# Kernel tuning notes

Measured on AMD Instinct MI355X. Metric: run time of the kernel, lower is better.

## Reference

```python
import jax, jax.numpy as jnp
import numpy as np

UNITS = 256
D_IN = 256


def setup_inputs() -> dict:
    key = jax.random.key(0)
    ks = jax.random.split(key, 12)
    B, T, M, d, u = 16, 128, 512, D_IN, UNITS
    s = lambda fan_in: 1.0 / np.sqrt(fan_in)
    return {
        "inputs": jax.random.normal(ks[0], (B, T, d), jnp.float32),
        "attended_inputs": jax.random.normal(ks[1], (B, M, d), jnp.float32),
        # key_dense: Dense(units) applied to attended_inputs
        "key_W": jax.random.normal(ks[2], (d, u), jnp.float32) * s(d),
        "key_b": jnp.zeros((u,), jnp.float32),
        # query_dense: Dense(units) applied to state_h
        "query_W": jax.random.normal(ks[3], (u, u), jnp.float32) * s(u),
        "query_b": jnp.zeros((u,), jnp.float32),
        # attention_dense: Dense(1)
        "attn_W": jax.random.normal(ks[4], (u, 1), jnp.float32) * s(u),
        "attn_b": jnp.zeros((1,), jnp.float32),
        # LSTMCell built with input dim 2*d (inputs concat context); gate order i,f,g,o
        "lstm_W": jax.random.normal(ks[5], (2 * d, 4 * u), jnp.float32) * s(2 * d),
        "lstm_U": jax.random.normal(ks[6], (u, 4 * u), jnp.float32) * s(u),
        "lstm_b": jnp.zeros((4 * u,), jnp.float32),
    }


def reference(inputs, attended_inputs, key_W, key_b, query_W, query_b,
              attn_W, attn_b, lstm_W, lstm_U, lstm_b):
    B, T, d = inputs.shape
    u = lstm_U.shape[0]
    # keys computed once, shared across all timesteps: [B, M, u]
    keys = jnp.einsum('bmd,du->bmu', attended_inputs, key_W) + key_b
    aw = attn_W[:, 0]  # [u]

    def step(carry, x_t):
        h, c = carry                                   # [B,u], [B,u]
        q = h @ query_W + query_b                      # [B,u]
        e = jnp.tanh(keys + q[:, None, :])             # [B,M,u]
        scores = jnp.einsum('bmu,u->bm', e, aw) + attn_b[0]
        a = jax.nn.softmax(scores, axis=-1)            # [B,M]
        ctx = jnp.einsum('bm,bmd->bd', a, attended_inputs)
        xin = jnp.concatenate([x_t, ctx], axis=-1)     # [B,2d]
        z = xin @ lstm_W + h @ lstm_U + lstm_b         # [B,4u]
        i_g, f_g, g_g, o_g = jnp.split(z, 4, axis=-1)
        i_g = jax.nn.sigmoid(i_g)
        f_g = jax.nn.sigmoid(f_g)
        g_g = jnp.tanh(g_g)
        o_g = jax.nn.sigmoid(o_g)
        c_new = f_g * c + i_g * g_g
        h_new = o_g * jnp.tanh(c_new)
        return (h_new, c_new), h_new

    h0 = jnp.zeros((B, u), inputs.dtype)
    c0 = jnp.zeros((B, u), inputs.dtype)
    (hT, cT), ys = jax.lax.scan(step, (h0, c0), jnp.swapaxes(inputs, 0, 1))
    seq = jnp.swapaxes(ys, 0, 1)  # [B,T,u] (return_sequences=True)
    return seq, hT, cT
```

## Files before the change

### kernel.cpp

```cpp
#include <hip/hip_runtime.h>
#include <hip/hip_bf16.h>
#include <cstddef>

#define BATCH 16
#define TSTEPS 128
#define MSLOTS 512
#define DIN 256
#define UNITS 256
#define ZDIM 1024
#define G 8
#define NBLK (BATCH*G)
#define NTHR 1024

static __device__ __forceinline__ float tanhf_fast(float x) {
    float e = __expf(2.0f * x);
    return 1.0f - 2.0f / (e + 1.0f);
}
static __device__ __forceinline__ float sigmoidf_fast(float x) {
    return 1.0f / (1.0f + __expf(-x));
}
static __device__ __forceinline__ void st_agent_u(unsigned* p, unsigned v) {
    __hip_atomic_store(p, v, __ATOMIC_RELAXED, __HIP_MEMORY_SCOPE_AGENT);
}
static __device__ __forceinline__ unsigned ld_agent_u(const unsigned* p) {
    return __hip_atomic_load(p, __ATOMIC_RELAXED, __HIP_MEMORY_SCOPE_AGENT);
}
static __device__ __forceinline__ unsigned pack_bf(float a, float b) {
    unsigned ua = __float_as_uint(a); ua = (ua + 0x7fffu + ((ua >> 16) & 1u)) >> 16;
    unsigned ub = __float_as_uint(b); ub = ((ub + 0x7fffu + ((ub >> 16) & 1u)) >> 16) << 16;
    return ua | ub;
}
static __device__ __forceinline__ float bf_lo(unsigned w) { return __uint_as_float(w << 16); }
static __device__ __forceinline__ float bf_hi(unsigned w) { return __uint_as_float(w & 0xffff0000u); }

__global__ __launch_bounds__(256) void gemm_bias_kernel(
    const float* __restrict__ A, const float* __restrict__ B,
    const float* __restrict__ bias, float* __restrict__ C,
    int M, int N, int K)
{
    __shared__ float As[16][68];
    __shared__ float Bs[16][68];
    const int tid = threadIdx.x;
    const int bm = blockIdx.x * 64;
    const int bn = blockIdx.y * 64;
    const int tx = tid & 15, ty = tid >> 4;
    const int ar = tid >> 2, ac = (tid & 3) * 4;
    const int br = tid >> 4, bc = (tid & 15) * 4;
    float acc[4][4] = {};

    for (int k0 = 0; k0 < K; k0 += 16) {
        float4 av = *(const float4*)(A + (size_t)(bm + ar) * K + k0 + ac);
        float4 bv = *(const float4*)(B + (size_t)(k0 + br) * N + bn + bc);
        As[ac + 0][ar] = av.x; As[ac + 1][ar] = av.y;
        As[ac + 2][ar] = av.z; As[ac + 3][ar] = av.w;
        *(float4*)(&Bs[br][bc]) = bv;
        __syncthreads();
#pragma unroll
        for (int kk = 0; kk < 16; ++kk) {
            float a0 = As[kk][ty*4+0], a1 = As[kk][ty*4+1];
            float a2 = As[kk][ty*4+2], a3 = As[kk][ty*4+3];
            float b0 = Bs[kk][tx*4+0], b1 = Bs[kk][tx*4+1];
            float b2 = Bs[kk][tx*4+2], b3 = Bs[kk][tx*4+3];
            acc[0][0]+=a0*b0; acc[0][1]+=a0*b1; acc[0][2]+=a0*b2; acc[0][3]+=a0*b3;
            acc[1][0]+=a1*b0; acc[1][1]+=a1*b1; acc[1][2]+=a1*b2; acc[1][3]+=a1*b3;
            acc[2][0]+=a2*b0; acc[2][1]+=a2*b1; acc[2][2]+=a2*b2; acc[2][3]+=a2*b3;
            acc[3][0]+=a3*b0; acc[3][1]+=a3*b1; acc[3][2]+=a3*b2; acc[3][3]+=a3*b3;
        }
        __syncthreads();
    }
#pragma unroll
    for (int i = 0; i < 4; ++i)
#pragma unroll
        for (int j = 0; j < 4; ++j) {
            int cn = bn + tx * 4 + j;
            C[(size_t)(bm + ty * 4 + i) * N + cn] = acc[i][j] + bias[cn];
        }
}

__global__ __launch_bounds__(256) void gemm_T_bf16_kernel(
    const float* __restrict__ A, const float* __restrict__ B,
    unsigned short* __restrict__ CT, int M, int N, int K)
{
    __shared__ float As[16][68];
    __shared__ float Bs[16][68];
    __shared__ float Ts[64][65];
    const int tid = threadIdx.x;
    const int bm = blockIdx.x * 64;
    const int bn = blockIdx.y * 64;
    const int tx = tid & 15, ty = tid >> 4;
    const int ar = tid >> 2, ac = (tid & 3) * 4;
    const int br = tid >> 4, bc = (tid & 15) * 4;
    float acc[4][4] = {};

    for (int k0 = 0; k0 < K; k0 += 16) {
        float4 av = *(const float4*)(A + (size_t)(bm + ar) * K + k0 + ac);
        float4 bv = *(const float4*)(B + (size_t)(k0 + br) * N + bn + bc);
        As[ac + 0][ar] = av.x; As[ac + 1][ar] = av.y;
        As[ac + 2][ar] = av.z; As[ac + 3][ar] = av.w;
        *(float4*)(&Bs[br][bc]) = bv;
        __syncthreads();
#pragma unroll
        for (int kk = 0; kk < 16; ++kk) {
            float a0 = As[kk][ty*4+0], a1 = As[kk][ty*4+1];
            float a2 = As[kk][ty*4+2], a3 = As[kk][ty*4+3];
            float b0 = Bs[kk][tx*4+0], b1 = Bs[kk][tx*4+1];
            float b2 = Bs[kk][tx*4+2], b3 = Bs[kk][tx*4+3];
            acc[0][0]+=a0*b0; acc[0][1]+=a0*b1; acc[0][2]+=a0*b2; acc[0][3]+=a0*b3;
            acc[1][0]+=a1*b0; acc[1][1]+=a1*b1; acc[1][2]+=a1*b2; acc[1][3]+=a1*b3;
            acc[2][0]+=a2*b0; acc[2][1]+=a2*b1; acc[2][2]+=a2*b2; acc[2][3]+=a2*b3;
            acc[3][0]+=a3*b0; acc[3][1]+=a3*b1; acc[3][2]+=a3*b2; acc[3][3]+=a3*b3;
        }
        __syncthreads();
    }
#pragma unroll
    for (int i = 0; i < 4; ++i)
#pragma unroll
        for (int j = 0; j < 4; ++j)
            Ts[tx * 4 + j][ty * 4 + i] = acc[i][j];
    __syncthreads();
    const int jr = tid >> 2, ms2 = (tid & 3) * 16;
    const int b = bm >> 9, m0 = bm & 511;
    unsigned short* dst = CT + (size_t)b * ((size_t)N * 512)
                        + (size_t)(bn + jr) * 512 + m0 + ms2;
#pragma unroll
    for (int u = 0; u < 16; ++u) {
        unsigned ua = __float_as_uint(Ts[jr][ms2 + u]);
        ua = (ua + 0x7fffu + ((ua >> 16) & 1u)) >> 16;
        dst[u] = (unsigned short)ua;
    }
}

__global__ __launch_bounds__(NTHR, 4) void rnn_persistent(
    const float* __restrict__ query_W, const float* __restrict__ query_b,
    const float* __restrict__ attn_W,  const float* __restrict__ lstm_U,
    const float* __restrict__ keys,    const float* __restrict__ pre,
    const unsigned short* __restrict__ aw2T,
    unsigned* pB, unsigned* hB, unsigned* sent,
    float* __restrict__ seq, float* __restrict__ hT, float* __restrict__ cT)
{
    const int bid = blockIdx.x;
    const int b = bid >> 3, g = bid & 7;
    const int tid = threadIdx.x;

    __shared__ unsigned aw2L[256 * 128];
    __shared__ __align__(16) float h_s[256];
    __shared__ __align__(16) float q_s[256];
    __shared__ __align__(16) float qp_s[4][256];
    __shared__ __align__(16) float p_s[512];
    __shared__ __align__(16) float pown_s[64];
    __shared__ __align__(16) float zp_s[8][128];
    __shared__ __align__(16) float z_s[128];
    __shared__ __align__(16) float aw_s[256];
    __shared__ __align__(16) float qb_s[256];
    __shared__ __align__(16) float red_s[8];

    const int jq = tid & 255, kq = tid >> 8;
    const int mloc = tid >> 4, jc = tid & 15;
    const int cc = tid & 127, ks = tid >> 7;
    const int col_own = ((cc >> 5) << 8) + g * 32 + (cc & 31);

    for (int i = tid; i < 256 * 128; i += NTHR) {
        int pr = i >> 7, c2 = i & 127;
        int colc = ((c2 >> 5) << 8) + g * 32 + (c2 & 31);
        aw2L[i] = ((const unsigned*)(aw2T + ((size_t)b * ZDIM + colc) * 512))[pr];
    }
    unsigned wq_r[32];
#pragma unroll
    for (int i = 0; i < 32; ++i)
        wq_r[i] = pack_bf(query_W[(size_t)(kq * 64 + 2 * i) * 256 + jq],
                          query_W[(size_t)(kq * 64 + 2 * i + 1) * 256 + jq]);
    unsigned keys_r[8];
    {
        const float* krow = keys + (size_t)(b * MSLOTS + g * 64 + mloc) * 256;
#pragma unroll
        for (int i = 0; i < 8; ++i)
            keys_r[i] = pack_bf(krow[jc + 32 * i], krow[jc + 32 * i + 16]);
    }
    unsigned u_r[16];
#pragma unroll
    for (int i = 0; i < 16; ++i)
        u_r[i] = pack_bf(lstm_U[(size_t)(ks * 32 + 2 * i) * ZDIM + col_own],
                         lstm_U[(size_t)(ks * 32 + 2 * i + 1) * ZDIM + col_own]);

    if (tid < 256) {
        aw_s[tid] = attn_W[tid];
        qb_s[tid] = query_b[tid];
        h_s[tid] = 0.0f;
    }
    float c_r = 0.0f;
    __syncthreads();

    const float* preb = pre + (size_t)b * TSTEPS * ZDIM;
    unsigned* pBb = pB + b * 512;
    unsigned* hBb = hB + b * 256;
    unsigned* sentb = sent + b * 16;

    for (int t = 0; t < TSTEPS; ++t) {
        const unsigned ptag = (unsigned)(2 * t + 1);
        const unsigned htag = (unsigned)(2 * t + 2);

        float pre_r = 0.0f;
        if (tid < 128)
            pre_r = preb[(size_t)t * ZDIM + col_own];

        {
            float qa = 0.0f;
#pragma unroll
            for (int i = 0; i < 32; ++i) {
                float2 hv = *(const float2*)&h_s[kq * 64 + 2 * i];
                qa += hv.x * bf_lo(wq_r[i]) + hv.y * bf_hi(wq_r[i]);
            }
            qp_s[kq][jq] = qa;
        }
        {
            float zh = 0.0f;
#pragma unroll
            for (int i = 0; i < 16; ++i) {
                float2 hv = *(const float2*)&h_s[ks * 32 + 2 * i];
                zh += hv.x * bf_lo(u_r[i]) + hv.y * bf_hi(u_r[i]);
            }
            zp_s[ks][cc] = zh;
        }
        __syncthreads();

        if (tid < 256)
            q_s[tid] = qb_s[tid] + qp_s[0][tid] + qp_s[1][tid] + qp_s[2][tid] + qp_s[3][tid];
        float zv = 0.0f;
        if (tid < 128)
            zv = pre_r + zp_s[0][cc] + zp_s[1][cc] + zp_s[2][cc] + zp_s[3][cc]
               + zp_s[4][cc] + zp_s[5][cc] + zp_s[6][cc] + zp_s[7][cc];
        __syncthreads();

        {
            float sacc = 0.0f;
#pragma unroll
            for (int i = 0; i < 8; ++i) {
                int j0 = jc + 32 * i, j1 = j0 + 16;
                unsigned kw = keys_r[i];
                sacc += aw_s[j0] * tanhf_fast(bf_lo(kw) + q_s[j0]);
                sacc += aw_s[j1] * tanhf_fast(bf_hi(kw) + q_s[j1]);
            }
            sacc += __shfl_xor(sacc, 1);
            sacc += __shfl_xor(sacc, 2);
            sacc += __shfl_xor(sacc, 4);
            sacc += __shfl_xor(sacc, 8);
            if (jc == 0) pown_s[mloc] = __expf(sacc);
        }
        __syncthreads();

        if (tid < 64) {
            st_agent_u(&pBb[g * 64 + tid], __float_as_uint(pown_s[tid]));
            asm volatile("s_waitcnt vmcnt(0)" ::: "memory");
            if (tid == 0) st_agent_u(&sentb[g], ptag);
        }
        if (tid < 8 && tid != g) {
            while (ld_agent_u(&sentb[tid]) < ptag)
                __builtin_amdgcn_s_sleep(1);
        }
        __syncthreads();
        if (tid < 512) {
            float pv;
            if ((tid >> 6) == g) pv = pown_s[tid & 63];
            else                 pv = __uint_as_float(ld_agent_u(&pBb[tid]));
            p_s[tid] = pv;
            float dv = pv;
            dv += __shfl_xor(dv, 1);  dv += __shfl_xor(dv, 2);  dv += __shfl_xor(dv, 4);
            dv += __shfl_xor(dv, 8);  dv += __shfl_xor(dv, 16); dv += __shfl_xor(dv, 32);
            if ((tid & 63) == 0) red_s[tid >> 6] = dv;
        }
        __syncthreads();
        float inv;
        {
            float tot = red_s[0] + red_s[1] + red_s[2] + red_s[3]
                      + red_s[4] + red_s[5] + red_s[6] + red_s[7];
            inv = 1.0f / tot;
        }

        {
            float zc = 0.0f;
#pragma unroll
            for (int i = 0; i < 32; ++i) {
                float2 pv = *(const float2*)&p_s[ks * 64 + 2 * i];
                unsigned w = aw2L[(ks * 32 + i) * 128 + cc];
                zc += pv.x * bf_lo(w) + pv.y * bf_hi(w);
            }
            zp_s[ks][cc] = zc;
        }
        __syncthreads();
        if (tid < 128) {
            float zcs = zp_s[0][cc] + zp_s[1][cc] + zp_s[2][cc] + zp_s[3][cc]
                      + zp_s[4][cc] + zp_s[5][cc] + zp_s[6][cc] + zp_s[7][cc];
            z_s[cc] = zv + zcs * inv;
        }
        __syncthreads();

        if (tid < 32) {
            float zi = z_s[tid], zf = z_s[32 + tid], zg = z_s[64 + tid], zo = z_s[96 + tid];
            float ig = sigmoidf_fast(zi);
            float fg = sigmoidf_fast(zf);
            float gg = tanhf_fast(zg);
            float og = sigmoidf_fast(zo);
            float cn = fg * c_r + ig * gg;
            float hn = og * tanhf_fast(cn);
            c_r = cn;
            int u = g * 32 + tid;
            h_s[u] = hn;
            st_agent_u(&hBb[u], __float_as_uint(hn));
            seq[((size_t)b * TSTEPS + t) * UNITS + u] = hn;
            if (t == TSTEPS - 1) { hT[b * UNITS + u] = hn; cT[b * UNITS + u] = cn; }
        }
        if (tid < 64) {
            asm volatile("s_waitcnt vmcnt(0)" ::: "memory");
            if (tid == 0) st_agent_u(&sentb[8 + g], htag);
        }
        if (tid < 8 && tid != g) {
            while (ld_agent_u(&sentb[8 + tid]) < htag)
                __builtin_amdgcn_s_sleep(1);
        }
        __syncthreads();
        if (tid < 256 && (tid >> 5) != g)
            h_s[tid] = __uint_as_float(ld_agent_u(&hBb[tid]));
        __syncthreads();
    }
}

extern "C" void kernel_launch(void* const* d_in, const int* in_sizes, int n_in,
                              void* d_out, int out_size, void* d_ws, size_t ws_size,
                              hipStream_t stream)
{
    (void)in_sizes; (void)n_in; (void)out_size; (void)ws_size;
    const float* inputs   = (const float*)d_in[0];
    const float* attended = (const float*)d_in[1];
    const float* key_W    = (const float*)d_in[2];
    const float* key_b    = (const float*)d_in[3];
    const float* query_W  = (const float*)d_in[4];
    const float* query_b  = (const float*)d_in[5];
    const float* attn_W   = (const float*)d_in[6];
    const float* lstm_W   = (const float*)d_in[8];
    const float* lstm_U   = (const float*)d_in[9];
    const float* lstm_b   = (const float*)d_in[10];

    float* out = (float*)d_out;
    float* seq = out;
    float* hT  = out + (size_t)BATCH * TSTEPS * UNITS;
    float* cT  = hT + BATCH * UNITS;

    float* ws = (float*)d_ws;
    float* keys = ws;
    float* pre  = keys + 2097152;
    unsigned short* aw2T = (unsigned short*)(pre + 2097152);
    unsigned* pB   = (unsigned*)(aw2T + (size_t)16 * 1024 * 512);
    unsigned* hB   = pB + BATCH * 512;
    unsigned* sent = hB + BATCH * 256;

    hipMemsetAsync(sent, 0, (size_t)BATCH * 16 * sizeof(unsigned), stream);

    gemm_bias_kernel<<<dim3(128, 4), 256, 0, stream>>>(
        attended, key_W, key_b, keys, 8192, 256, 256);
    gemm_bias_kernel<<<dim3(32, 16), 256, 0, stream>>>(
        inputs, lstm_W, lstm_b, pre, 2048, 1024, 256);
    gemm_T_bf16_kernel<<<dim3(128, 16), 256, 0, stream>>>(
        attended, lstm_W + (size_t)256 * ZDIM, aw2T, 8192, 1024, 256);

    rnn_persistent<<<dim3(NBLK), dim3(NTHR), 0, stream>>>(
        query_W, query_b, attn_W, lstm_U,
        keys, pre, aw2T, pB, hB, sent, seq, hT, cT);
}
```

Measured before the change: 1.607 ms.

## Embed step tags in exchanged values to drop separate flag barriers

Replaces the separate sentinel flags with an 8-bit step tag packed into the low mantissa bits of each exchanged p and h value. Consumers poll each value directly, which removes the store-wait-flag round trips and the extra block barriers. The recurrent U-matrix partial product is moved after the attention scores so it can hide the exchange latency. In exchange, h and p lose 8 mantissa bits (h is truncated even in the seq output), and correctness relies on the tag not wrapping ambiguously and on initialising the buffers to 0xFF.

```diff
diff --git a/kernel.cpp b/kernel.cpp
--- a/kernel.cpp
+++ b/kernel.cpp
@@ -24,6 +24,14 @@
 }
 static __device__ __forceinline__ unsigned ld_agent_u(const unsigned* p) {
     return __hip_atomic_load(p, __ATOMIC_RELAXED, __HIP_MEMORY_SCOPE_AGENT);
+}
+static __device__ __forceinline__ float poll_tag(const unsigned* p, unsigned tag) {
+    unsigned w = ld_agent_u(p);
+    while ((w & 0xFFu) != tag) {
+        __builtin_amdgcn_s_sleep(1);
+        w = ld_agent_u(p);
+    }
+    return __uint_as_float(w & 0xFFFFFF00u);
 }
 static __device__ __forceinline__ unsigned pack_bf(float a, float b) {
     unsigned ua = __float_as_uint(a); ua = (ua + 0x7fffu + ((ua >> 16) & 1u)) >> 16;
@@ -135,7 +143,7 @@
     const float* __restrict__ attn_W,  const float* __restrict__ lstm_U,
     const float* __restrict__ keys,    const float* __restrict__ pre,
     const unsigned short* __restrict__ aw2T,
-    unsigned* pB, unsigned* hB, unsigned* sent,
+    unsigned* pB, unsigned* hB,
     float* __restrict__ seq, float* __restrict__ hT, float* __restrict__ cT)
 {
     const int bid = blockIdx.x;
@@ -193,11 +201,10 @@
     const float* preb = pre + (size_t)b * TSTEPS * ZDIM;
     unsigned* pBb = pB + b * 512;
     unsigned* hBb = hB + b * 256;
-    unsigned* sentb = sent + b * 16;
 
     for (int t = 0; t < TSTEPS; ++t) {
-        const unsigned ptag = (unsigned)(2 * t + 1);
-        const unsigned htag = (unsigned)(2 * t + 2);
+        const unsigned ptag = (unsigned)((2 * t + 1) & 0xFF);
+        const unsigned htag = (unsigned)((2 * t + 2) & 0xFF);
 
         float pre_r = 0.0f;
         if (tid < 128)
@@ -212,23 +219,9 @@
             }
             qp_s[kq][jq] = qa;
         }
-        {
-            float zh = 0.0f;
-#pragma unroll
-            for (int i = 0; i < 16; ++i) {
-                float2 hv = *(const float2*)&h_s[ks * 32 + 2 * i];
-                zh += hv.x * bf_lo(u_r[i]) + hv.y * bf_hi(u_r[i]);
-            }
-            zp_s[ks][cc] = zh;
-        }
-        __syncthreads();
-
+        __syncthreads();
         if (tid < 256)
             q_s[tid] = qb_s[tid] + qp_s[0][tid] + qp_s[1][tid] + qp_s[2][tid] + qp_s[3][tid];
-        float zv = 0.0f;
-        if (tid < 128)
-            zv = pre_r + zp_s[0][cc] + zp_s[1][cc] + zp_s[2][cc] + zp_s[3][cc]
-               + zp_s[4][cc] + zp_s[5][cc] + zp_s[6][cc] + zp_s[7][cc];
         __syncthreads();
 
         {
@@ -244,24 +237,33 @@
             sacc += __shfl_xor(sacc, 2);
             sacc += __shfl_xor(sacc, 4);
             sacc += __shfl_xor(sacc, 8);
-            if (jc == 0) pown_s[mloc] = __expf(sacc);
-        }
-        __syncthreads();
-
-        if (tid < 64) {
-            st_agent_u(&pBb[g * 64 + tid], __float_as_uint(pown_s[tid]));
-            asm volatile("s_waitcnt vmcnt(0)" ::: "memory");
-            if (tid == 0) st_agent_u(&sentb[g], ptag);
-        }
-        if (tid < 8 && tid != g) {
-            while (ld_agent_u(&sentb[tid]) < ptag)
-                __builtin_amdgcn_s_sleep(1);
-        }
-        __syncthreads();
+            if (jc == 0) {
+                float pv = __expf(sacc);
+                unsigned w = (__float_as_uint(pv) & 0xFFFFFF00u) | ptag;
+                pown_s[mloc] = __uint_as_float(w & 0xFFFFFF00u);
+                st_agent_u(&pBb[g * 64 + mloc], w);
+            }
+        }
+
+        {
+            float zh = 0.0f;
+#pragma unroll
+            for (int i = 0; i < 16; ++i) {
+                float2 hv = *(const float2*)&h_s[ks * 32 + 2 * i];
+                zh += hv.x * bf_lo(u_r[i]) + hv.y * bf_hi(u_r[i]);
+            }
+            zp_s[ks][cc] = zh;
+        }
+        __syncthreads();
+
+        float zv = 0.0f;
+        if (tid < 128)
+            zv = pre_r + zp_s[0][cc] + zp_s[1][cc] + zp_s[2][cc] + zp_s[3][cc]
+               + zp_s[4][cc] + zp_s[5][cc] + zp_s[6][cc] + zp_s[7][cc];
         if (tid < 512) {
             float pv;
             if ((tid >> 6) == g) pv = pown_s[tid & 63];
-            else                 pv = __uint_as_float(ld_agent_u(&pBb[tid]));
+            else                 pv = poll_tag(&pBb[tid], ptag);
             p_s[tid] = pv;
             float dv = pv;
             dv += __shfl_xor(dv, 1);  dv += __shfl_xor(dv, 2);  dv += __shfl_xor(dv, 4);
@@ -303,23 +305,17 @@
             float cn = fg * c_r + ig * gg;
             float hn = og * tanhf_fast(cn);
             c_r = cn;
+            unsigned w = (__float_as_uint(hn) & 0xFFFFFF00u) | htag;
+            float hn_t = __uint_as_float(w & 0xFFFFFF00u);
             int u = g * 32 + tid;
-            h_s[u] = hn;
-            st_agent_u(&hBb[u], __float_as_uint(hn));
-            seq[((size_t)b * TSTEPS + t) * UNITS + u] = hn;
-            if (t == TSTEPS - 1) { hT[b * UNITS + u] = hn; cT[b * UNITS + u] = cn; }
-        }
-        if (tid < 64) {
-            asm volatile("s_waitcnt vmcnt(0)" ::: "memory");
-            if (tid == 0) st_agent_u(&sentb[8 + g], htag);
-        }
-        if (tid < 8 && tid != g) {
-            while (ld_agent_u(&sentb[8 + tid]) < htag)
-                __builtin_amdgcn_s_sleep(1);
-        }
-        __syncthreads();
+            h_s[u] = hn_t;
+            st_agent_u(&hBb[u], w);
+            seq[((size_t)b * TSTEPS + t) * UNITS + u] = hn_t;
+            if (t == TSTEPS - 1) { hT[b * UNITS + u] = hn_t; cT[b * UNITS + u] = cn; }
+        }
+
         if (tid < 256 && (tid >> 5) != g)
-            h_s[tid] = __uint_as_float(ld_agent_u(&hBb[tid]));
+            h_s[tid] = poll_tag(&hBb[tid], htag);
         __syncthreads();
     }
 }
@@ -349,11 +345,10 @@
     float* keys = ws;
     float* pre  = keys + 2097152;
     unsigned short* aw2T = (unsigned short*)(pre + 2097152);
-    unsigned* pB   = (unsigned*)(aw2T + (size_t)16 * 1024 * 512);
-    unsigned* hB   = pB + BATCH * 512;
-    unsigned* sent = hB + BATCH * 256;
-
-    hipMemsetAsync(sent, 0, (size_t)BATCH * 16 * sizeof(unsigned), stream);
+    unsigned* pB = (unsigned*)(aw2T + (size_t)16 * 1024 * 512);
+    unsigned* hB = pB + BATCH * 512;
+
+    hipMemsetAsync(pB, 0xFF, (size_t)BATCH * (512 + 256) * sizeof(unsigned), stream);
 
     gemm_bias_kernel<<<dim3(128, 4), 256, 0, stream>>>(
         attended, key_W, key_b, keys, 8192, 256, 256);
@@ -364,5 +359,5 @@
 
     rnn_persistent<<<dim3(NBLK), dim3(NTHR), 0, stream>>>(
         query_W, query_b, attn_W, lstm_U,
-        keys, pre, aw2T, pB, hB, sent, seq, hT, cT);
-}
+        keys, pre, aw2T, pB, hB, seq, hT, cT);
+}
```

Result: slower. 1.769 ms (+10.1%).

## Regroup persistent RNN blocks into 16-block groups each handling two batch rows

Applied to the files above, without the earlier changes.

The persistent recurrent kernel now assigns each group of 16 blocks to two batch rows, instead of 8 blocks per batch row. Each block owns 32 attention slots and 16 hidden units per row. It computes the attention scores for both rows in sequence and publishes them with per-row flags, overlapping that publication with the recurrent h·U product. This halves each block's share of work per row, but it adds extra block barriers and twice as many peer flags to poll per step. Grid-wide synchronisation latency may therefore dominate.

```diff
diff --git a/kernel.cpp b/kernel.cpp
--- a/kernel.cpp
+++ b/kernel.cpp
@@ -8,8 +8,9 @@
 #define DIN 256
 #define UNITS 256
 #define ZDIM 1024
-#define G 8
-#define NBLK (BATCH*G)
+#define GROUPS 8
+#define GBLK 16
+#define NBLK (GROUPS*GBLK)
 #define NTHR 1024
 
 static __device__ __forceinline__ float tanhf_fast(float x) {
@@ -139,42 +140,47 @@
     float* __restrict__ seq, float* __restrict__ hT, float* __restrict__ cT)
 {
     const int bid = blockIdx.x;
-    const int b = bid >> 3, g = bid & 7;
+    const int grp = bid & 7, gb = bid >> 3;
+    const int b0 = grp * 2;
     const int tid = threadIdx.x;
 
-    __shared__ unsigned aw2L[256 * 128];
-    __shared__ __align__(16) float h_s[256];
+    __shared__ unsigned aw2L[2][256 * 64];
+    __shared__ __align__(16) float h_s[2][256];
     __shared__ __align__(16) float q_s[256];
     __shared__ __align__(16) float qp_s[4][256];
-    __shared__ __align__(16) float p_s[512];
-    __shared__ __align__(16) float pown_s[64];
+    __shared__ __align__(16) float p_s[1024];
+    __shared__ __align__(16) float pown_s[2][32];
     __shared__ __align__(16) float zp_s[8][128];
+    __shared__ __align__(16) float zhsum_s[128];
     __shared__ __align__(16) float z_s[128];
     __shared__ __align__(16) float aw_s[256];
     __shared__ __align__(16) float qb_s[256];
-    __shared__ __align__(16) float red_s[8];
+    __shared__ __align__(16) float red_s[16];
 
     const int jq = tid & 255, kq = tid >> 8;
-    const int mloc = tid >> 4, jc = tid & 15;
-    const int cc = tid & 127, ks = tid >> 7;
-    const int col_own = ((cc >> 5) << 8) + g * 32 + (cc & 31);
-
-    for (int i = tid; i < 256 * 128; i += NTHR) {
-        int pr = i >> 7, c2 = i & 127;
-        int colc = ((c2 >> 5) << 8) + g * 32 + (c2 & 31);
-        aw2L[i] = ((const unsigned*)(aw2T + ((size_t)b * ZDIM + colc) * 512))[pr];
+    const int mloc = tid >> 5, jc = tid & 31;
+    const int cc2 = tid & 127, ks = tid >> 7;
+    const int bt_z = cc2 >> 6, cc = cc2 & 63;
+    const int col_own = ((cc >> 4) << 8) + gb * 16 + (cc & 15);
+
+    for (int i = tid; i < 2 * 256 * 64; i += NTHR) {
+        int bt = i >> 14, r = i & 16383;
+        int pr = r >> 6, c2 = r & 63;
+        int colc = ((c2 >> 4) << 8) + gb * 16 + (c2 & 15);
+        aw2L[bt][r] = ((const unsigned*)(aw2T + ((size_t)(b0 + bt) * ZDIM + colc) * 512))[pr];
     }
     unsigned wq_r[32];
 #pragma unroll
     for (int i = 0; i < 32; ++i)
         wq_r[i] = pack_bf(query_W[(size_t)(kq * 64 + 2 * i) * 256 + jq],
                           query_W[(size_t)(kq * 64 + 2 * i + 1) * 256 + jq]);
-    unsigned keys_r[8];
-    {
-        const float* krow = keys + (size_t)(b * MSLOTS + g * 64 + mloc) * 256;
-#pragma unroll
-        for (int i = 0; i < 8; ++i)
-            keys_r[i] = pack_bf(krow[jc + 32 * i], krow[jc + 32 * i + 16]);
+    unsigned keys_r[2][4];
+#pragma unroll
+    for (int bt = 0; bt < 2; ++bt) {
+        const float* krow = keys + (size_t)((b0 + bt) * MSLOTS + gb * 32 + mloc) * 256;
+#pragma unroll
+        for (int i = 0; i < 4; ++i)
+            keys_r[bt][i] = pack_bf(krow[jc + 64 * i], krow[jc + 64 * i + 32]);
     }
     unsigned u_r[16];
 #pragma unroll
@@ -185,83 +191,94 @@
     if (tid < 256) {
         aw_s[tid] = attn_W[tid];
         qb_s[tid] = query_b[tid];
-        h_s[tid] = 0.0f;
+        h_s[0][tid] = 0.0f;
+        h_s[1][tid] = 0.0f;
     }
     float c_r = 0.0f;
     __syncthreads();
 
-    const float* preb = pre + (size_t)b * TSTEPS * ZDIM;
-    unsigned* pBb = pB + b * 512;
-    unsigned* hBb = hB + b * 256;
-    unsigned* sentb = sent + b * 16;
+    unsigned* sentP0 = sent + grp * 64;
+    unsigned* sentP1 = sentP0 + 16;
+    unsigned* sentH0 = sentP0 + 32;
+    unsigned* sentH1 = sentP0 + 48;
 
     for (int t = 0; t < TSTEPS; ++t) {
-        const unsigned ptag = (unsigned)(2 * t + 1);
-        const unsigned htag = (unsigned)(2 * t + 2);
+        const unsigned tag = (unsigned)(t + 1);
 
         float pre_r = 0.0f;
         if (tid < 128)
-            pre_r = preb[(size_t)t * ZDIM + col_own];
-
-        {
-            float qa = 0.0f;
-#pragma unroll
-            for (int i = 0; i < 32; ++i) {
-                float2 hv = *(const float2*)&h_s[kq * 64 + 2 * i];
-                qa += hv.x * bf_lo(wq_r[i]) + hv.y * bf_hi(wq_r[i]);
-            }
-            qp_s[kq][jq] = qa;
-        }
+            pre_r = pre[((size_t)(b0 + bt_z) * TSTEPS + t) * ZDIM + col_own];
+
+#pragma unroll
+        for (int bt = 0; bt < 2; ++bt) {
+            {
+                float qa = 0.0f;
+#pragma unroll
+                for (int i = 0; i < 32; ++i) {
+                    float2 hv = *(const float2*)&h_s[bt][kq * 64 + 2 * i];
+                    qa += hv.x * bf_lo(wq_r[i]) + hv.y * bf_hi(wq_r[i]);
+                }
+                qp_s[kq][jq] = qa;
+            }
+            __syncthreads();
+            if (tid < 256)
+                q_s[tid] = qb_s[tid] + qp_s[0][tid] + qp_s[1][tid]
+                         + qp_s[2][tid] + qp_s[3][tid];
+            __syncthreads();
+            {
+                float sacc = 0.0f;
+#pragma unroll
+                for (int i = 0; i < 4; ++i) {
+                    int j0 = jc + 64 * i, j1 = j0 + 32;
+                    unsigned kw = keys_r[bt][i];
+                    sacc += aw_s[j0] * tanhf_fast(bf_lo(kw) + q_s[j0]);
+                    sacc += aw_s[j1] * tanhf_fast(bf_hi(kw) + q_s[j1]);
+                }
+                sacc += __shfl_xor(sacc, 1);
+                sacc += __shfl_xor(sacc, 2);
+                sacc += __shfl_xor(sacc, 4);
+                sacc += __shfl_xor(sacc, 8);
+                sacc += __shfl_xor(sacc, 16);
+                if (jc == 0) pown_s[bt][mloc] = __expf(sacc);
+            }
+            __syncthreads();
+            if (tid < 64) {
+                if (tid < 32)
+                    st_agent_u(&pB[(size_t)(b0 + bt) * 512 + gb * 32 + tid],
+                               __float_as_uint(pown_s[bt][tid]));
+                asm volatile("s_waitcnt vmcnt(0)" ::: "memory");
+                if (tid == 0) st_agent_u(bt ? &sentP1[gb] : &sentP0[gb], tag);
+            }
+        }
+
         {
             float zh = 0.0f;
 #pragma unroll
             for (int i = 0; i < 16; ++i) {
-                float2 hv = *(const float2*)&h_s[ks * 32 + 2 * i];
+                float2 hv = *(const float2*)&h_s[bt_z][ks * 32 + 2 * i];
                 zh += hv.x * bf_lo(u_r[i]) + hv.y * bf_hi(u_r[i]);
             }
-            zp_s[ks][cc] = zh;
-        }
-        __syncthreads();
-
-        if (tid < 256)
-            q_s[tid] = qb_s[tid] + qp_s[0][tid] + qp_s[1][tid] + qp_s[2][tid] + qp_s[3][tid];
-        float zv = 0.0f;
+            zp_s[ks][cc2] = zh;
+        }
+        __syncthreads();
         if (tid < 128)
-            zv = pre_r + zp_s[0][cc] + zp_s[1][cc] + zp_s[2][cc] + zp_s[3][cc]
-               + zp_s[4][cc] + zp_s[5][cc] + zp_s[6][cc] + zp_s[7][cc];
+            zhsum_s[tid] = pre_r + zp_s[0][tid] + zp_s[1][tid] + zp_s[2][tid]
+                         + zp_s[3][tid] + zp_s[4][tid] + zp_s[5][tid]
+                         + zp_s[6][tid] + zp_s[7][tid];
+        if (tid < 16) {
+            if (tid != gb)
+                while (ld_agent_u(&sentP0[tid]) < tag) __builtin_amdgcn_s_sleep(1);
+        } else if (tid < 32) {
+            if ((tid & 15) != gb)
+                while (ld_agent_u(&sentP1[tid & 15]) < tag) __builtin_amdgcn_s_sleep(1);
+        }
         __syncthreads();
 
         {
-            float sacc = 0.0f;
-#pragma unroll
-            for (int i = 0; i < 8; ++i) {
-                int j0 = jc + 32 * i, j1 = j0 + 16;
-                unsigned kw = keys_r[i];
-                sacc += aw_s[j0] * tanhf_fast(bf_lo(kw) + q_s[j0]);
-                sacc += aw_s[j1] * tanhf_fast(bf_hi(kw) + q_s[j1]);
-            }
-            sacc += __shfl_xor(sacc, 1);
-            sacc += __shfl_xor(sacc, 2);
-            sacc += __shfl_xor(sacc, 4);
-            sacc += __shfl_xor(sacc, 8);
-            if (jc == 0) pown_s[mloc] = __expf(sacc);
-        }
-        __syncthreads();
-
-        if (tid < 64) {
-            st_agent_u(&pBb[g * 64 + tid], __float_as_uint(pown_s[tid]));
-            asm volatile("s_waitcnt vmcnt(0)" ::: "memory");
-            if (tid == 0) st_agent_u(&sentb[g], ptag);
-        }
-        if (tid < 8 && tid != g) {
-            while (ld_agent_u(&sentb[tid]) < ptag)
-                __builtin_amdgcn_s_sleep(1);
-        }
-        __syncthreads();
-        if (tid < 512) {
+            int btg = tid >> 9, idx = tid & 511;
             float pv;
-            if ((tid >> 6) == g) pv = pown_s[tid & 63];
-            else                 pv = __uint_as_float(ld_agent_u(&pBb[tid]));
+            if ((idx >> 5) == gb) pv = pown_s[btg][idx & 31];
+            else pv = __uint_as_float(ld_agent_u(&pB[(size_t)(b0 + btg) * 512 + idx]));
             p_s[tid] = pv;
             float dv = pv;
             dv += __shfl_xor(dv, 1);  dv += __shfl_xor(dv, 2);  dv += __shfl_xor(dv, 4);
@@ -269,33 +286,38 @@
             if ((tid & 63) == 0) red_s[tid >> 6] = dv;
         }
         __syncthreads();
-        float inv;
+        float inv0, inv1;
         {
-            float tot = red_s[0] + red_s[1] + red_s[2] + red_s[3]
-                      + red_s[4] + red_s[5] + red_s[6] + red_s[7];
-            inv = 1.0f / tot;
+            float t0 = red_s[0] + red_s[1] + red_s[2] + red_s[3]
+                     + red_s[4] + red_s[5] + red_s[6] + red_s[7];
+            float t1 = red_s[8] + red_s[9] + red_s[10] + red_s[11]
+                     + red_s[12] + red_s[13] + red_s[14] + red_s[15];
+            inv0 = 1.0f / t0;
+            inv1 = 1.0f / t1;
         }
 
         {
             float zc = 0.0f;
 #pragma unroll
             for (int i = 0; i < 32; ++i) {
-                float2 pv = *(const float2*)&p_s[ks * 64 + 2 * i];
-                unsigned w = aw2L[(ks * 32 + i) * 128 + cc];
+                float2 pv = *(const float2*)&p_s[bt_z * 512 + ks * 64 + 2 * i];
+                unsigned w = aw2L[bt_z][(ks * 32 + i) * 64 + cc];
                 zc += pv.x * bf_lo(w) + pv.y * bf_hi(w);
             }
-            zp_s[ks][cc] = zc;
+            zp_s[ks][cc2] = zc;
         }
         __syncthreads();
         if (tid < 128) {
-            float zcs = zp_s[0][cc] + zp_s[1][cc] + zp_s[2][cc] + zp_s[3][cc]
-                      + zp_s[4][cc] + zp_s[5][cc] + zp_s[6][cc] + zp_s[7][cc];
-            z_s[cc] = zv + zcs * inv;
+            float zcs = zp_s[0][tid] + zp_s[1][tid] + zp_s[2][tid] + zp_s[3][tid]
+                      + zp_s[4][tid] + zp_s[5][tid] + zp_s[6][tid] + zp_s[7][tid];
+            z_s[tid] = zhsum_s[tid] + zcs * (bt_z ? inv1 : inv0);
         }
         __syncthreads();
 
         if (tid < 32) {
-            float zi = z_s[tid], zf = z_s[32 + tid], zg = z_s[64 + tid], zo = z_s[96 + tid];
+            int bt = tid >> 4, ul = tid & 15, base = bt * 64;
+            float zi = z_s[base + ul],      zf = z_s[base + 16 + ul];
+            float zg = z_s[base + 32 + ul], zo = z_s[base + 48 + ul];
             float ig = sigmoidf_fast(zi);
             float fg = sigmoidf_fast(zf);
             float gg = tanhf_fast(zg);
@@ -303,23 +325,35 @@
             float cn = fg * c_r + ig * gg;
             float hn = og * tanhf_fast(cn);
             c_r = cn;
-            int u = g * 32 + tid;
-            h_s[u] = hn;
-            st_agent_u(&hBb[u], __float_as_uint(hn));
-            seq[((size_t)b * TSTEPS + t) * UNITS + u] = hn;
-            if (t == TSTEPS - 1) { hT[b * UNITS + u] = hn; cT[b * UNITS + u] = cn; }
+            int u = gb * 16 + ul;
+            h_s[bt][u] = hn;
+            st_agent_u(&hB[(size_t)(b0 + bt) * 256 + u], __float_as_uint(hn));
+            seq[((size_t)(b0 + bt) * TSTEPS + t) * UNITS + u] = hn;
+            if (t == TSTEPS - 1) {
+                hT[(b0 + bt) * UNITS + u] = hn;
+                cT[(b0 + bt) * UNITS + u] = cn;
+            }
         }
         if (tid < 64) {
             asm volatile("s_waitcnt vmcnt(0)" ::: "memory");
-            if (tid == 0) st_agent_u(&sentb[8 + g], htag);
-        }
-        if (tid < 8 && tid != g) {
-            while (ld_agent_u(&sentb[8 + tid]) < htag)
-                __builtin_amdgcn_s_sleep(1);
-        }
-        __syncthreads();
-        if (tid < 256 && (tid >> 5) != g)
-            h_s[tid] = __uint_as_float(ld_agent_u(&hBb[tid]));
+            if (tid == 0) st_agent_u(&sentH0[gb], tag);
+            if (tid == 1) st_agent_u(&sentH1[gb], tag);
+        }
+
+        if (tid < 16) {
+            if (tid != gb)
+                while (ld_agent_u(&sentH0[tid]) < tag) __builtin_amdgcn_s_sleep(1);
+        } else if (tid < 32) {
+            if ((tid & 15) != gb)
+                while (ld_agent_u(&sentH1[tid & 15]) < tag) __builtin_amdgcn_s_sleep(1);
+        }
+        __syncthreads();
+        if (tid < 512) {
+            int bt = tid >> 8, u2 = tid & 255;
+            if ((u2 >> 4) != gb)
+                h_s[bt][u2] = __uint_as_float(
+                    ld_agent_u(&hB[(size_t)(b0 + bt) * 256 + u2]));
+        }
         __syncthreads();
     }
 }
@@ -353,7 +387,7 @@
     unsigned* hB   = pB + BATCH * 512;
     unsigned* sent = hB + BATCH * 256;
 
-    hipMemsetAsync(sent, 0, (size_t)BATCH * 16 * sizeof(unsigned), stream);
+    hipMemsetAsync(sent, 0, (size_t)GROUPS * 64 * sizeof(unsigned), stream);
 
     gemm_bias_kernel<<<dim3(128, 4), 256, 0, stream>>>(
         attended, key_W, key_b, keys, 8192, 256, 256);
```

Result: slower. 2.294 ms (+42.8%).
